# Optimization experiments

Hardware: AMD Instinct MI355X
Metric: run time of the kernel (lower is better)

Reference implementation:

```python
import jax, jax.numpy as jnp
import numpy as np

L = 15      # GNN layers
D = 128     # hidden width


def _mlp3(x, w1, b1, w2, b2, w3, b3):
    h = jax.nn.relu(x @ w1 + b1)
    h = jax.nn.relu(h @ w2 + b2)
    return h @ w3 + b3


def _layernorm(x, g, b, eps=1e-5):
    mu = x.mean(-1, keepdims=True)
    var = ((x - mu) ** 2).mean(-1, keepdims=True)
    return (x - mu) / jnp.sqrt(var + eps) * g + b


def _gather(V, idx):
    # V: [B,N,D], idx: [B,E] -> [B,E,D]
    return jax.vmap(lambda v, i: v[i])(V, idx)


def _scatter_sum(e, idx, n):
    # e: [B,E,D], idx: [B,E] -> [B,n,D]
    return jax.vmap(lambda ee, ii: jnp.zeros((n, ee.shape[-1]), ee.dtype).at[ii].add(ee))(e, idx)


def setup_inputs() -> dict:
    key = jax.random.key(0)
    ks = iter(jax.random.split(key, 64))
    B, N, Eg = 1, 10000, 40000

    def lin(fi, fo, pre=()):
        s = 1.0 / np.sqrt(fi)
        w = jax.random.uniform(next(ks), pre + (fi, fo), jnp.float32, -s, s)
        b = jax.random.uniform(next(ks), pre + (fo,), jnp.float32, -s, s)
        return w, b

    inp = {}
    inp['node_pos'] = jax.random.normal(next(ks), (B, N, 3), jnp.float32)
    inp['areas'] = jax.random.uniform(next(ks), (B, N, 1), jnp.float32)
    inp['info'] = jax.random.normal(next(ks), (B, 1, 8), jnp.float32)
    inp['edges'] = jax.random.randint(next(ks), (B, Eg, 2), 0, N, jnp.int32)

    # Encoder MLPs (layer_norm=True)
    for pre, fi in [('fv', 12), ('fe', 4)]:
        w1, b1 = lin(fi, D); w2, b2 = lin(D, D); w3, b3 = lin(D, D)
        inp[pre + '_w1'], inp[pre + '_b1'] = w1, b1
        inp[pre + '_w2'], inp[pre + '_b2'] = w2, b2
        inp[pre + '_w3'], inp[pre + '_b3'] = w3, b3
        inp[pre + '_g'] = jnp.ones((D,), jnp.float32)
        inp[pre + '_bt'] = jnp.zeros((D,), jnp.float32)

    # 15 GNN layers, stacked along leading axis (layer_norm=False)
    for pre, fi in [('ge', D + 2 * D), ('gn', D + D)]:
        w1, b1 = lin(fi, D, (L,)); w2, b2 = lin(D, D, (L,)); w3, b3 = lin(D, D, (L,))
        inp[pre + '_w1'], inp[pre + '_b1'] = w1, b1
        inp[pre + '_w2'], inp[pre + '_b2'] = w2, b2
        inp[pre + '_w3'], inp[pre + '_b3'] = w3, b3

    # Decoder (layer_norm=False, output_size=1)
    w1, b1 = lin(D, D); w2, b2 = lin(D, D); w3, b3 = lin(D, 1)
    inp['de_w1'], inp['de_b1'] = w1, b1
    inp['de_w2'], inp['de_b2'] = w2, b2
    inp['de_w3'], inp['de_b3'] = w3, b3
    return inp


def reference(node_pos, areas, info, edges,
              fv_w1, fv_b1, fv_w2, fv_b2, fv_w3, fv_b3, fv_g, fv_bt,
              fe_w1, fe_b1, fe_w2, fe_b2, fe_w3, fe_b3, fe_g, fe_bt,
              ge_w1, ge_b1, ge_w2, ge_b2, ge_w3, ge_b3,
              gn_w1, gn_b1, gn_w2, gn_b2, gn_w3, gn_b3,
              de_w1, de_b1, de_w2, de_b2, de_w3, de_b3):
    B, N, _ = node_pos.shape
    info_b = jnp.broadcast_to(info, (B, N, info.shape[-1]))
    en_in = jnp.concatenate([node_pos, areas, info_b], -1)  # [B,N,12]

    s, r = edges[..., 0], edges[..., 1]
    dist = _gather(node_pos, s) - _gather(node_pos, r)      # [B,E,3]
    nrm = jnp.sqrt((dist ** 2).sum(-1, keepdims=True))
    E_raw = jnp.concatenate([dist, nrm], -1)                # [B,E,4]

    V = _layernorm(_mlp3(en_in, fv_w1, fv_b1, fv_w2, fv_b2, fv_w3, fv_b3), fv_g, fv_bt)
    E = _layernorm(_mlp3(E_raw, fe_w1, fe_b1, fe_w2, fe_b2, fe_w3, fe_b3), fe_g, fe_bt)

    def step(carry, p):
        V, E = carry
        w1, b1, w2, b2, w3, b3, nw1, nb1, nw2, nb2, nw3, nb3 = p
        e_in = jnp.concatenate([_gather(V, s), _gather(V, r), E], -1)  # [B,E,384]
        e_emb = _mlp3(e_in, w1, b1, w2, b2, w3, b3)
        agg = _scatter_sum(e_emb, s, N)                                # [B,N,128]
        v_emb = _mlp3(jnp.concatenate([V, agg], -1), nw1, nb1, nw2, nb2, nw3, nb3)
        return (V + v_emb, E + e_emb), None

    (V, E), _ = jax.lax.scan(step, (V, E),
                             (ge_w1, ge_b1, ge_w2, ge_b2, ge_w3, ge_b3,
                              gn_w1, gn_b1, gn_w2, gn_b2, gn_w3, gn_b3))

    return _mlp3(V, de_w1, de_b1, de_w2, de_b2, de_w3, de_b3)  # [B,N,1]
```

## Files before the change

### kernel.cpp

```cpp
#include <hip/hip_runtime.h>

#define DD 128
#define N_NODE 10000
#define N_EDGE 40000
#define N_LAYER 15

typedef unsigned short U16;
typedef __attribute__((ext_vector_type(8))) short short8;
typedef __attribute__((ext_vector_type(4))) float f32x4;

enum { A_BF16 = 0, A_EDGE, A_NODE, A_ENCIN, A_ERAW };
enum { EPI_F = 0, EPI_EDGE, EPI_NODE, EPI_DEC };

#define OFF_FV1 0
#define OFF_FV2 4096
#define OFF_FV3 20480
#define OFF_FE1 36864
#define OFF_FE2 40960
#define OFF_FE3 57344
#define OFF_GE1 73728
#define OFF_GE2 811008
#define OFF_GE3 1056768
#define OFF_GN1 1302528
#define OFF_GN2 1794048
#define OFF_GN3 2039808
#define OFF_DE1 2285568
#define OFF_DE2 2301952
#define WT_TOTAL 2318336

static __device__ __forceinline__ U16 f2b(float f) {
    union { float f; unsigned u; } x; x.f = f;
    unsigned u = x.u;
    return (U16)((u + 0x7fffu + ((u >> 16) & 1u)) >> 16);
}
static __device__ __forceinline__ float b2f(U16 u) {
    union { unsigned u; float f; } x; x.u = ((unsigned)u) << 16;
    return x.f;
}

static __device__ __forceinline__ void wgb() {
    __asm__ __volatile__("s_waitcnt lgkmcnt(0)\n\ts_barrier" ::: "memory");
}

struct I4x2 { int4 a, b; };

__global__ __launch_bounds__(256)
void wprep(const float* fv1, const float* fv2, const float* fv3,
           const float* fe1, const float* fe2, const float* fe3,
           const float* ge1, const float* ge2, const float* ge3,
           const float* gn1, const float* gn2, const float* gn3,
           const float* de1, const float* de2, U16* Wt)
{
    int b = blockIdx.x;
    const float* src; U16* dst; int K, Kpad, k0;
    if      (b < 1)   { src = fv1; K = 12;  Kpad = 32;  dst = Wt + OFF_FV1; k0 = b * 32; }
    else if (b < 5)   { src = fv2; K = 128; Kpad = 128; dst = Wt + OFF_FV2; k0 = (b-1)*32; }
    else if (b < 9)   { src = fv3; K = 128; Kpad = 128; dst = Wt + OFF_FV3; k0 = (b-5)*32; }
    else if (b < 10)  { src = fe1; K = 4;   Kpad = 32;  dst = Wt + OFF_FE1; k0 = (b-9)*32; }
    else if (b < 14)  { src = fe2; K = 128; Kpad = 128; dst = Wt + OFF_FE2; k0 = (b-10)*32; }
    else if (b < 18)  { src = fe3; K = 128; Kpad = 128; dst = Wt + OFF_FE3; k0 = (b-14)*32; }
    else if (b < 198) { int r = b-18,  mi = r/12, s = r%12; src = ge1 + (size_t)mi*384*128; K = 384; Kpad = 384; dst = Wt + OFF_GE1 + (size_t)mi*49152; k0 = s*32; }
    else if (b < 258) { int r = b-198, mi = r/4,  s = r%4;  src = ge2 + (size_t)mi*16384;   K = 128; Kpad = 128; dst = Wt + OFF_GE2 + (size_t)mi*16384; k0 = s*32; }
    else if (b < 318) { int r = b-258, mi = r/4,  s = r%4;  src = ge3 + (size_t)mi*16384;   K = 128; Kpad = 128; dst = Wt + OFF_GE3 + (size_t)mi*16384; k0 = s*32; }
    else if (b < 438) { int r = b-318, mi = r/8,  s = r%8;  src = gn1 + (size_t)mi*32768;   K = 256; Kpad = 256; dst = Wt + OFF_GN1 + (size_t)mi*32768; k0 = s*32; }
    else if (b < 498) { int r = b-438, mi = r/4,  s = r%4;  src = gn2 + (size_t)mi*16384;   K = 128; Kpad = 128; dst = Wt + OFF_GN2 + (size_t)mi*16384; k0 = s*32; }
    else if (b < 558) { int r = b-498, mi = r/4,  s = r%4;  src = gn3 + (size_t)mi*16384;   K = 128; Kpad = 128; dst = Wt + OFF_GN3 + (size_t)mi*16384; k0 = s*32; }
    else if (b < 562) { src = de1; K = 128; Kpad = 128; dst = Wt + OFF_DE1; k0 = (b-558)*32; }
    else              { src = de2; K = 128; Kpad = 128; dst = Wt + OFF_DE2; k0 = (b-562)*32; }

    __shared__ float T[32][129];
    #pragma unroll
    for (int i = 0; i < 16; ++i) {
        int l = threadIdx.x + i * 256;
        int kk = l >> 7, n = l & 127;
        int kg = k0 + kk;
        T[kk][n] = (kg < K) ? src[(size_t)kg * 128 + n] : 0.f;
    }
    __syncthreads();
    int n = threadIdx.x >> 1, h = threadIdx.x & 1;
    union { U16 u[16]; int4 v[2]; } o;
    #pragma unroll
    for (int j = 0; j < 16; ++j) o.u[j] = f2b(T[h * 16 + j][n]);
    int4* d = (int4*)(dst + (size_t)n * Kpad + k0 + h * 16);
    d[0] = o.v[0]; d[1] = o.v[1];
}

__global__ __launch_bounds__(256)
void csr_hist(const int* __restrict__ edges, int* __restrict__ cnt, int Eg)
{
    int e = blockIdx.x * 256 + threadIdx.x;
    if (e < Eg) atomicAdd(&cnt[edges[2 * e]], 1);
}

__global__ __launch_bounds__(256)
void csr_scan(const int* __restrict__ cnt, int* __restrict__ rowptr,
              int* __restrict__ cursor, int n)
{
    __shared__ int ps[256];
    int t = threadIdx.x, base = t * 40;
    int s = 0;
    for (int j = 0; j < 40; ++j) if (base + j < n) s += cnt[base + j];
    ps[t] = s; __syncthreads();
    for (int off = 1; off < 256; off <<= 1) {
        int v = (t >= off) ? ps[t - off] : 0;
        __syncthreads();
        ps[t] += v;
        __syncthreads();
    }
    int run = ps[t] - s;
    for (int j = 0; j < 40; ++j) {
        if (base + j < n) {
            rowptr[base + j] = run;
            cursor[base + j] = run;
            run += cnt[base + j];
        }
    }
    if (t == 255) rowptr[n] = ps[255];
}

__global__ __launch_bounds__(256)
void csr_scatter(const int* __restrict__ edges, int* __restrict__ cursor,
                 int* __restrict__ spos, int Eg)
{
    int e = blockIdx.x * 256 + threadIdx.x;
    if (e < Eg) spos[e] = atomicAdd(&cursor[edges[2 * e]], 1);
}

template<int ASRC, int EPI, int K1>
__global__ __launch_bounds__(256)
void mlp3(const U16* __restrict__ Af,
          const U16* __restrict__ W1, const float* __restrict__ b1,
          const U16* __restrict__ W2, const float* __restrict__ b2,
          const U16* __restrict__ W3, const float* __restrict__ b3,
          U16* __restrict__ outh, float* __restrict__ outf,
          const int* __restrict__ edges, const int* __restrict__ rowptr,
          const int* __restrict__ spos, float* __restrict__ eEs,
          const U16* __restrict__ Vh, const U16* __restrict__ Ehp,
          const float* __restrict__ pos, const float* __restrict__ area,
          const float* __restrict__ info, const float* __restrict__ w3f,
          int M)
{
    __shared__ U16 As[2][64][40];
    __shared__ U16 Bs[2][128][40];
    __shared__ U16 Hs[64][132];

    const int tid  = threadIdx.x;
    const int row0 = blockIdx.x * 64;
    const int wave = tid >> 6, lane = tid & 63;
    const int quad = lane >> 4, l16 = lane & 15;
    const int wm = (wave >> 1) * 32;
    const int wn = (wave & 1) * 64;
    const int sr = tid >> 2, sh = tid & 3;
    const int br = tid >> 1, bh = tid & 1;
    const int sm = row0 + sr;
    const bool valid = (sm < M);

    int si = 0, ri = 0, jbeg = 0, jend = 0;
    if ((ASRC == A_EDGE || ASRC == A_ERAW) && valid) {
        si = edges[2 * sm]; ri = edges[2 * sm + 1];
    }
    if (ASRC == A_NODE && valid) { jbeg = rowptr[sm]; jend = rowptr[sm + 1]; }

    f32x4 acc[4][2];

    auto zacc = [&] {
        #pragma unroll
        for (int i = 0; i < 4; ++i)
            #pragma unroll
            for (int j = 0; j < 2; ++j) acc[i][j] = (f32x4)0.f;
    };

    auto ldA = [&](int c) -> int4 {
        if (ASRC == A_ENCIN || ASRC == A_ERAW) {
            union { U16 u[8]; int4 v; } pk;
            #pragma unroll
            for (int j = 0; j < 8; ++j) pk.u[j] = 0;
            if (valid) {
                if (ASRC == A_ENCIN) {
                    #pragma unroll
                    for (int j = 0; j < 8; ++j) {
                        int col = sh * 8 + j;
                        float x = 0.f;
                        if (col < 3)       x = pos[3 * sm + col];
                        else if (col == 3) x = area[sm];
                        else if (col < 12) x = info[col - 4];
                        pk.u[j] = f2b(x);
                    }
                } else if (sh == 0) {
                    float dx = pos[3*si]   - pos[3*ri];
                    float dy = pos[3*si+1] - pos[3*ri+1];
                    float dz = pos[3*si+2] - pos[3*ri+2];
                    float nm = sqrtf(dx*dx + dy*dy + dz*dz);
                    pk.u[0] = f2b(dx); pk.u[1] = f2b(dy);
                    pk.u[2] = f2b(dz); pk.u[3] = f2b(nm);
                }
            }
            return pk.v;
        } else if (ASRC == A_NODE && c >= 4) {
            float a[8];
            #pragma unroll
            for (int i = 0; i < 8; ++i) a[i] = 0.f;
            if (valid) {
                const float* base = eEs + (c - 4) * 32 + sh * 8;
                for (int j = jbeg; j < jend; ++j) {
                    const float4* r = (const float4*)(base + (size_t)j * 128);
                    float4 x0 = r[0], x1 = r[1];
                    a[0]+=x0.x; a[1]+=x0.y; a[2]+=x0.z; a[3]+=x0.w;
                    a[4]+=x1.x; a[5]+=x1.y; a[6]+=x1.z; a[7]+=x1.w;
                }
            }
            union { U16 u[8]; int4 v; } pk;
            #pragma unroll
            for (int i = 0; i < 8; ++i) pk.u[i] = f2b(a[i]);
            return pk.v;
        } else {
            const U16* s;
            if (ASRC == A_BF16)        s = Af + (size_t)sm * K1 + c * 32;
            else if (ASRC == A_EDGE) {
                if (c < 4)             s = Vh  + (size_t)si * 128 + c * 32;
                else if (c < 8)        s = Vh  + (size_t)ri * 128 + (c - 4) * 32;
                else                   s = Ehp + (size_t)sm * 128 + (c - 8) * 32;
            } else                     s = Vh  + (size_t)sm * 128 + c * 32;
            return valid ? *(const int4*)(s + sh * 8) : make_int4(0,0,0,0);
        }
    };

    auto ldW = [&](const U16* W, int Kw, int c) -> I4x2 {
        const U16* s = W + (size_t)br * Kw + c * 32 + bh * 16;
        I4x2 r;
        r.a = ((const int4*)s)[0];
        r.b = ((const int4*)s)[1];
        return r;
    };

    auto wrA = [&](int b, int4 v) { *(int4*)&As[b][sr][sh * 8] = v; };
    auto wrW = [&](int b, I4x2 w) {
        *(int4*)&Bs[b][br][bh * 16]     = w.a;
        *(int4*)&Bs[b][br][bh * 16 + 8] = w.b;
    };

    auto mfA = [&](int b) {
        short8 wf[4], af[2];
        #pragma unroll
        for (int g = 0; g < 4; ++g)
            wf[g] = *(const short8*)&Bs[b][wn + g*16 + l16][quad * 8];
        #pragma unroll
        for (int g = 0; g < 2; ++g)
            af[g] = *(const short8*)&As[b][wm + g*16 + l16][quad * 8];
        #pragma unroll
        for (int wg = 0; wg < 4; ++wg)
            #pragma unroll
            for (int ag = 0; ag < 2; ++ag)
                acc[wg][ag] = __builtin_amdgcn_mfma_f32_16x16x32_bf16(
                    wf[wg], af[ag], acc[wg][ag], 0, 0, 0);
    };

    auto mfH = [&](int c, int b) {
        short8 wf[4], af[2];
        #pragma unroll
        for (int g = 0; g < 4; ++g)
            wf[g] = *(const short8*)&Bs[b][wn + g*16 + l16][quad * 8];
        #pragma unroll
        for (int g = 0; g < 2; ++g)
            af[g] = *(const short8*)&Hs[wm + g*16 + l16][c * 32 + quad * 8];
        #pragma unroll
        for (int wg = 0; wg < 4; ++wg)
            #pragma unroll
            for (int ag = 0; ag < 2; ++ag)
                acc[wg][ag] = __builtin_amdgcn_mfma_f32_16x16x32_bf16(
                    wf[wg], af[ag], acc[wg][ag], 0, 0, 0);
    };

    auto hwrite = [&](const float* bias) {
        #pragma unroll
        for (int wg = 0; wg < 4; ++wg) {
            f32x4 bv = *(const f32x4*)&bias[wn + wg*16 + quad*4];
            #pragma unroll
            for (int ag = 0; ag < 2; ++ag) {
                int m  = wm + ag*16 + l16;
                int n0 = wn + wg*16 + quad*4;
                union { U16 u[4]; uint2 q; } pk;
                #pragma unroll
                for (int rg = 0; rg < 4; ++rg)
                    pk.u[rg] = f2b(fmaxf(acc[wg][ag][rg] + bv[rg], 0.f));
                *(uint2*)&Hs[m][n0] = pk.q;
            }
        }
    };

    int4 ra0, ra1; I4x2 rw0, rw1;
    constexpr int C1 = K1 / 32;

    zacc();
    ra0 = ldA(0); rw0 = ldW(W1, K1, 0);
    if (C1 > 1) { ra1 = ldA(1); rw1 = ldW(W1, K1, 1); }
    wrA(0, ra0); wrW(0, rw0);
    wgb();
    #pragma unroll
    for (int c = 0; c < C1; ++c) {
        if (c + 2 < C1) {
            if ((c & 1) == 0) { ra0 = ldA(c + 2); rw0 = ldW(W1, K1, c + 2); }
            else              { ra1 = ldA(c + 2); rw1 = ldW(W1, K1, c + 2); }
        }
        if (c + 1 < C1) {
            if (((c + 1) & 1) == 0) { wrA(0, ra0); wrW(0, rw0); }
            else                    { wrA(1, ra1); wrW(1, rw1); }
        }
        mfA(c & 1);
        wgb();
    }

    rw0 = ldW(W2, 128, 0); rw1 = ldW(W2, 128, 1);
    hwrite(b1);
    wgb();
    zacc();
    wrW(0, rw0);
    wgb();
    #pragma unroll
    for (int c = 0; c < 4; ++c) {
        if (c + 2 < 4) {
            if ((c & 1) == 0) rw0 = ldW(W2, 128, c + 2);
            else              rw1 = ldW(W2, 128, c + 2);
        }
        if (c + 1 < 4) {
            if (((c + 1) & 1) == 0) wrW(0, rw0);
            else                    wrW(1, rw1);
        }
        mfH(c, c & 1);
        wgb();
    }

    if (EPI == EPI_DEC) {
        hwrite(b2);
        wgb();
        int mg = row0 + sr;
        float v = 0.f;
        if (mg < M) {
            const U16* hr = &Hs[sr][sh * 32];
            const float* wr = w3f + sh * 32;
            #pragma unroll
            for (int j = 0; j < 32; ++j) v += b2f(hr[j]) * wr[j];
        }
        v += __shfl_xor(v, 1);
        v += __shfl_xor(v, 2);
        if (sh == 0 && mg < M) outf[mg] = v + b3[0];
        return;
    }

    rw0 = ldW(W3, 128, 0); rw1 = ldW(W3, 128, 1);
    hwrite(b2);
    wgb();
    zacc();
    wrW(0, rw0);
    wgb();
    #pragma unroll
    for (int c = 0; c < 4; ++c) {
        if (c + 2 < 4) {
            if ((c & 1) == 0) rw0 = ldW(W3, 128, c + 2);
            else              rw1 = ldW(W3, 128, c + 2);
        }
        if (c + 1 < 4) {
            if (((c + 1) & 1) == 0) wrW(0, rw0);
            else                    wrW(1, rw1);
        }
        mfH(c, c & 1);
        wgb();
    }

    f32x4 bvs[4];
    #pragma unroll
    for (int wg = 0; wg < 4; ++wg)
        bvs[wg] = *(const f32x4*)&b3[wn + wg*16 + quad*4];
    #pragma unroll
    for (int ag = 0; ag < 2; ++ag) {
        int mg = row0 + wm + ag*16 + l16;
        if (mg >= M) continue;
        int sp = 0;
        if (EPI == EPI_EDGE) sp = spos[mg];
        #pragma unroll
        for (int wg = 0; wg < 4; ++wg) {
            int n0 = wn + wg*16 + quad*4;
            f32x4 v;
            #pragma unroll
            for (int rg = 0; rg < 4; ++rg) v[rg] = acc[wg][ag][rg] + bvs[wg][rg];
            size_t o = (size_t)mg * 128 + n0;
            if (EPI == EPI_F) {
                *(f32x4*)&outf[o] = v;
            } else {
                f32x4 c = *(f32x4*)&outf[o];
                c += v;
                *(f32x4*)&outf[o] = c;
                union { U16 u[4]; uint2 q; } pk;
                #pragma unroll
                for (int rg = 0; rg < 4; ++rg) pk.u[rg] = f2b(c[rg]);
                *(uint2*)&outh[o] = pk.q;
                if (EPI == EPI_EDGE)
                    *(f32x4*)&eEs[(size_t)sp * 128 + n0] = v;
            }
        }
    }
}

__global__ __launch_bounds__(256)
void ln_kernel(float* __restrict__ X, const float* __restrict__ g,
               const float* __restrict__ b, U16* __restrict__ Xh, int rows)
{
    int row  = blockIdx.x * 4 + (threadIdx.x >> 6);
    int lane = threadIdx.x & 63;
    if (row >= rows) return;
    float x0 = X[row * DD + lane];
    float x1 = X[row * DD + 64 + lane];
    float s = x0 + x1, q = x0 * x0 + x1 * x1;
    #pragma unroll
    for (int off = 32; off; off >>= 1) {
        s += __shfl_xor(s, off);
        q += __shfl_xor(q, off);
    }
    float mu  = s * (1.f / 128.f);
    float var = q * (1.f / 128.f) - mu * mu;
    float inv = rsqrtf(var + 1e-5f);
    float y0 = (x0 - mu) * inv * g[lane]      + b[lane];
    float y1 = (x1 - mu) * inv * g[64 + lane] + b[64 + lane];
    X[row * DD + lane]       = y0;
    X[row * DD + 64 + lane]  = y1;
    Xh[row * DD + lane]      = f2b(y0);
    Xh[row * DD + 64 + lane] = f2b(y1);
}

extern "C" void kernel_launch(void* const* d_in, const int* in_sizes, int n_in,
                              void* d_out, int out_size, void* d_ws, size_t ws_size,
                              hipStream_t stream)
{
    (void)in_sizes; (void)n_in; (void)out_size; (void)ws_size;

    const float* pos   = (const float*)d_in[0];
    const float* area  = (const float*)d_in[1];
    const float* info  = (const float*)d_in[2];
    const int*   edges = (const int*)d_in[3];
    const float* fv_w1 = (const float*)d_in[4];
    const float* fv_b1 = (const float*)d_in[5];
    const float* fv_w2 = (const float*)d_in[6];
    const float* fv_b2 = (const float*)d_in[7];
    const float* fv_w3 = (const float*)d_in[8];
    const float* fv_b3 = (const float*)d_in[9];
    const float* fv_g  = (const float*)d_in[10];
    const float* fv_bt = (const float*)d_in[11];
    const float* fe_w1 = (const float*)d_in[12];
    const float* fe_b1 = (const float*)d_in[13];
    const float* fe_w2 = (const float*)d_in[14];
    const float* fe_b2 = (const float*)d_in[15];
    const float* fe_w3 = (const float*)d_in[16];
    const float* fe_b3 = (const float*)d_in[17];
    const float* fe_g  = (const float*)d_in[18];
    const float* fe_bt = (const float*)d_in[19];
    const float* ge_w1 = (const float*)d_in[20];
    const float* ge_b1 = (const float*)d_in[21];
    const float* ge_w2 = (const float*)d_in[22];
    const float* ge_b2 = (const float*)d_in[23];
    const float* ge_w3 = (const float*)d_in[24];
    const float* ge_b3 = (const float*)d_in[25];
    const float* gn_w1 = (const float*)d_in[26];
    const float* gn_b1 = (const float*)d_in[27];
    const float* gn_w2 = (const float*)d_in[28];
    const float* gn_b2 = (const float*)d_in[29];
    const float* gn_w3 = (const float*)d_in[30];
    const float* gn_b3 = (const float*)d_in[31];
    const float* de_w1 = (const float*)d_in[32];
    const float* de_b1 = (const float*)d_in[33];
    const float* de_w2 = (const float*)d_in[34];
    const float* de_b2 = (const float*)d_in[35];
    const float* de_w3 = (const float*)d_in[36];
    const float* de_b3 = (const float*)d_in[37];

    char* p = (char*)d_ws;
    float* Vf   = (float*)p;  p += (size_t)N_NODE * 128 * 4;
    float* Ef   = (float*)p;  p += (size_t)N_EDGE * 128 * 4;
    float* eEs  = (float*)p;  p += (size_t)N_EDGE * 128 * 4;
    U16*  Vh    = (U16*)p;    p += (size_t)N_NODE * 128 * 2;
    U16*  Eh    = (U16*)p;    p += (size_t)N_EDGE * 128 * 2;
    U16*  Wt    = (U16*)p;    p += (size_t)WT_TOTAL * 2;
    int*  rowptr = (int*)p;   p += (size_t)(N_NODE + 4) * 4;
    int*  cursor = (int*)p;   p += (size_t)N_NODE * 4;
    int*  cnt    = (int*)p;   p += (size_t)N_NODE * 4;
    int*  spos   = (int*)p;   p += (size_t)N_EDGE * 4;

    const int gbE = (N_EDGE + 63) / 64;
    const int gbN = (N_NODE + 63) / 64;

    wprep<<<566, 256, 0, stream>>>(fv_w1, fv_w2, fv_w3, fe_w1, fe_w2, fe_w3,
                                   ge_w1, ge_w2, ge_w3, gn_w1, gn_w2, gn_w3,
                                   de_w1, de_w2, Wt);
    hipMemsetAsync(cnt, 0, (size_t)N_NODE * 4, stream);
    csr_hist<<<(N_EDGE + 255) / 256, 256, 0, stream>>>(edges, cnt, N_EDGE);
    csr_scan<<<1, 256, 0, stream>>>(cnt, rowptr, cursor, N_NODE);
    csr_scatter<<<(N_EDGE + 255) / 256, 256, 0, stream>>>(edges, cursor, spos, N_EDGE);

    mlp3<A_ERAW, EPI_F, 32><<<gbE, 256, 0, stream>>>(
        nullptr, Wt + OFF_FE1, fe_b1, Wt + OFF_FE2, fe_b2, Wt + OFF_FE3, fe_b3,
        nullptr, Ef, edges, nullptr, nullptr, nullptr, nullptr, nullptr,
        pos, nullptr, nullptr, nullptr, N_EDGE);
    ln_kernel<<<(N_EDGE + 3) / 4, 256, 0, stream>>>(Ef, fe_g, fe_bt, Eh, N_EDGE);

    mlp3<A_ENCIN, EPI_F, 32><<<gbN, 256, 0, stream>>>(
        nullptr, Wt + OFF_FV1, fv_b1, Wt + OFF_FV2, fv_b2, Wt + OFF_FV3, fv_b3,
        nullptr, Vf, nullptr, nullptr, nullptr, nullptr, nullptr, nullptr,
        pos, area, info, nullptr, N_NODE);
    ln_kernel<<<(N_NODE + 3) / 4, 256, 0, stream>>>(Vf, fv_g, fv_bt, Vh, N_NODE);

    for (int l = 0; l < N_LAYER; ++l) {
        mlp3<A_EDGE, EPI_EDGE, 384><<<gbE, 256, 0, stream>>>(
            nullptr,
            Wt + OFF_GE1 + (size_t)l * 49152, ge_b1 + (size_t)l * 128,
            Wt + OFF_GE2 + (size_t)l * 16384, ge_b2 + (size_t)l * 128,
            Wt + OFF_GE3 + (size_t)l * 16384, ge_b3 + (size_t)l * 128,
            Eh, Ef, edges, nullptr, spos, eEs, Vh, Eh,
            nullptr, nullptr, nullptr, nullptr, N_EDGE);
        mlp3<A_NODE, EPI_NODE, 256><<<gbN, 256, 0, stream>>>(
            nullptr,
            Wt + OFF_GN1 + (size_t)l * 32768, gn_b1 + (size_t)l * 128,
            Wt + OFF_GN2 + (size_t)l * 16384, gn_b2 + (size_t)l * 128,
            Wt + OFF_GN3 + (size_t)l * 16384, gn_b3 + (size_t)l * 128,
            Vh, Vf, nullptr, rowptr, nullptr, eEs, Vh, nullptr,
            nullptr, nullptr, nullptr, nullptr, N_NODE);
    }

    mlp3<A_BF16, EPI_DEC, 128><<<gbN, 256, 0, stream>>>(
        Vh, Wt + OFF_DE1, de_b1, Wt + OFF_DE2, de_b2, nullptr, de_b3,
        nullptr, (float*)d_out, nullptr, nullptr, nullptr, nullptr, nullptr, nullptr,
        nullptr, nullptr, nullptr, de_w3, N_NODE);
}
```

Before: 1.094 ms.

## Move MLP kernels to 512-thread blocks and shrink node tiles to 32 rows

Each fused MLP block now runs 8 waves instead of 4, with the wave grid changed to 2x4 over a BM x 128 tile so each wave does fewer MFMAs per K-chunk. The row tile is templated: edge kernels keep 64 rows, while node, encoder and decoder kernels use 32 rows, doubling their grid size. The aim is more waves in flight to hide gather and global-load latency, and better CU fill for the 10k-node kernels. The cost is less weight reuse per block, extra barrier participants, and some threads left idle when staging A tiles.

After: 1.027 ms (median of 2 runs). 1.06x faster.

```diff
diff --git a/kernel.cpp b/kernel.cpp
--- a/kernel.cpp
+++ b/kernel.cpp
@@ -41,8 +41,6 @@
 static __device__ __forceinline__ void wgb() {
     __asm__ __volatile__("s_waitcnt lgkmcnt(0)\n\ts_barrier" ::: "memory");
 }
-
-struct I4x2 { int4 a, b; };
 
 __global__ __launch_bounds__(256)
 void wprep(const float* fv1, const float* fv2, const float* fv3,
@@ -126,8 +124,8 @@
     if (e < Eg) spos[e] = atomicAdd(&cursor[edges[2 * e]], 1);
 }
 
-template<int ASRC, int EPI, int K1>
-__global__ __launch_bounds__(256)
+template<int ASRC, int EPI, int K1, int BM>
+__global__ __launch_bounds__(512, 4)
 void mlp3(const U16* __restrict__ Af,
           const U16* __restrict__ W1, const float* __restrict__ b1,
           const U16* __restrict__ W2, const float* __restrict__ b2,
@@ -140,20 +138,22 @@
           const float* __restrict__ info, const float* __restrict__ w3f,
           int M)
 {
-    __shared__ U16 As[2][64][40];
+    constexpr int NAG = BM / 32;
+    __shared__ U16 As[2][BM][40];
     __shared__ U16 Bs[2][128][40];
-    __shared__ U16 Hs[64][132];
+    __shared__ U16 Hs[BM][132];
 
     const int tid  = threadIdx.x;
-    const int row0 = blockIdx.x * 64;
+    const int row0 = blockIdx.x * BM;
     const int wave = tid >> 6, lane = tid & 63;
     const int quad = lane >> 4, l16 = lane & 15;
-    const int wm = (wave >> 1) * 32;
-    const int wn = (wave & 1) * 64;
+    const int wm = (wave >> 2) * (16 * NAG);
+    const int wn = (wave & 3) * 32;
     const int sr = tid >> 2, sh = tid & 3;
-    const int br = tid >> 1, bh = tid & 1;
+    const int br = tid >> 2, bh = tid & 3;
     const int sm = row0 + sr;
-    const bool valid = (sm < M);
+    const bool stager = (tid < BM * 4);
+    const bool valid  = stager && (sm < M);
 
     int si = 0, ri = 0, jbeg = 0, jend = 0;
     if ((ASRC == A_EDGE || ASRC == A_ERAW) && valid) {
@@ -161,13 +161,13 @@
     }
     if (ASRC == A_NODE && valid) { jbeg = rowptr[sm]; jend = rowptr[sm + 1]; }
 
-    f32x4 acc[4][2];
+    f32x4 acc[2][NAG];
 
     auto zacc = [&] {
         #pragma unroll
-        for (int i = 0; i < 4; ++i)
-            #pragma unroll
-            for (int j = 0; j < 2; ++j) acc[i][j] = (f32x4)0.f;
+        for (int i = 0; i < 2; ++i)
+            #pragma unroll
+            for (int j = 0; j < NAG; ++j) acc[i][j] = (f32x4)0.f;
     };
 
     auto ldA = [&](int c) -> int4 {
@@ -225,58 +225,52 @@
         }
     };
 
-    auto ldW = [&](const U16* W, int Kw, int c) -> I4x2 {
-        const U16* s = W + (size_t)br * Kw + c * 32 + bh * 16;
-        I4x2 r;
-        r.a = ((const int4*)s)[0];
-        r.b = ((const int4*)s)[1];
-        return r;
+    auto ldW = [&](const U16* W, int Kw, int c) -> int4 {
+        const U16* s = W + (size_t)br * Kw + c * 32 + bh * 8;
+        return *(const int4*)s;
     };
 
-    auto wrA = [&](int b, int4 v) { *(int4*)&As[b][sr][sh * 8] = v; };
-    auto wrW = [&](int b, I4x2 w) {
-        *(int4*)&Bs[b][br][bh * 16]     = w.a;
-        *(int4*)&Bs[b][br][bh * 16 + 8] = w.b;
-    };
+    auto wrA = [&](int b, int4 v) { if (stager) *(int4*)&As[b][sr][sh * 8] = v; };
+    auto wrW = [&](int b, int4 w) { *(int4*)&Bs[b][br][bh * 8] = w; };
 
     auto mfA = [&](int b) {
-        short8 wf[4], af[2];
-        #pragma unroll
-        for (int g = 0; g < 4; ++g)
+        short8 wf[2], af[NAG];
+        #pragma unroll
+        for (int g = 0; g < 2; ++g)
             wf[g] = *(const short8*)&Bs[b][wn + g*16 + l16][quad * 8];
         #pragma unroll
-        for (int g = 0; g < 2; ++g)
+        for (int g = 0; g < NAG; ++g)
             af[g] = *(const short8*)&As[b][wm + g*16 + l16][quad * 8];
         #pragma unroll
-        for (int wg = 0; wg < 4; ++wg)
-            #pragma unroll
-            for (int ag = 0; ag < 2; ++ag)
+        for (int wg = 0; wg < 2; ++wg)
+            #pragma unroll
+            for (int ag = 0; ag < NAG; ++ag)
                 acc[wg][ag] = __builtin_amdgcn_mfma_f32_16x16x32_bf16(
                     wf[wg], af[ag], acc[wg][ag], 0, 0, 0);
     };
 
     auto mfH = [&](int c, int b) {
-        short8 wf[4], af[2];
-        #pragma unroll
-        for (int g = 0; g < 4; ++g)
+        short8 wf[2], af[NAG];
+        #pragma unroll
+        for (int g = 0; g < 2; ++g)
             wf[g] = *(const short8*)&Bs[b][wn + g*16 + l16][quad * 8];
         #pragma unroll
-        for (int g = 0; g < 2; ++g)
+        for (int g = 0; g < NAG; ++g)
             af[g] = *(const short8*)&Hs[wm + g*16 + l16][c * 32 + quad * 8];
         #pragma unroll
-        for (int wg = 0; wg < 4; ++wg)
-            #pragma unroll
-            for (int ag = 0; ag < 2; ++ag)
+        for (int wg = 0; wg < 2; ++wg)
+            #pragma unroll
+            for (int ag = 0; ag < NAG; ++ag)
                 acc[wg][ag] = __builtin_amdgcn_mfma_f32_16x16x32_bf16(
                     wf[wg], af[ag], acc[wg][ag], 0, 0, 0);
     };
 
     auto hwrite = [&](const float* bias) {
         #pragma unroll
-        for (int wg = 0; wg < 4; ++wg) {
+        for (int wg = 0; wg < 2; ++wg) {
             f32x4 bv = *(const f32x4*)&bias[wn + wg*16 + quad*4];
             #pragma unroll
-            for (int ag = 0; ag < 2; ++ag) {
+            for (int ag = 0; ag < NAG; ++ag) {
                 int m  = wm + ag*16 + l16;
                 int n0 = wn + wg*16 + quad*4;
                 union { U16 u[4]; uint2 q; } pk;
@@ -288,7 +282,7 @@
         }
     };
 
-    int4 ra0, ra1; I4x2 rw0, rw1;
+    int4 ra0, ra1, rw0, rw1;
     constexpr int C1 = K1 / 32;
 
     zacc();
@@ -333,17 +327,20 @@
     if (EPI == EPI_DEC) {
         hwrite(b2);
         wgb();
-        int mg = row0 + sr;
+        constexpr int TPR = 512 / BM;
+        constexpr int CPT = 128 / TPR;
+        int r = tid / TPR, s8 = tid % TPR;
+        int mg = row0 + r;
         float v = 0.f;
         if (mg < M) {
-            const U16* hr = &Hs[sr][sh * 32];
-            const float* wr = w3f + sh * 32;
-            #pragma unroll
-            for (int j = 0; j < 32; ++j) v += b2f(hr[j]) * wr[j];
-        }
-        v += __shfl_xor(v, 1);
-        v += __shfl_xor(v, 2);
-        if (sh == 0 && mg < M) outf[mg] = v + b3[0];
+            const U16* hr = &Hs[r][s8 * CPT];
+            const float* wr = w3f + s8 * CPT;
+            #pragma unroll
+            for (int j = 0; j < CPT; ++j) v += b2f(hr[j]) * wr[j];
+        }
+        #pragma unroll
+        for (int off = 1; off < TPR; off <<= 1) v += __shfl_xor(v, off);
+        if (s8 == 0 && mg < M) outf[mg] = v + b3[0];
         return;
     }
 
@@ -367,18 +364,18 @@
         wgb();
     }
 
-    f32x4 bvs[4];
-    #pragma unroll
-    for (int wg = 0; wg < 4; ++wg)
+    f32x4 bvs[2];
+    #pragma unroll
+    for (int wg = 0; wg < 2; ++wg)
         bvs[wg] = *(const f32x4*)&b3[wn + wg*16 + quad*4];
     #pragma unroll
-    for (int ag = 0; ag < 2; ++ag) {
+    for (int ag = 0; ag < NAG; ++ag) {
         int mg = row0 + wm + ag*16 + l16;
         if (mg >= M) continue;
         int sp = 0;
         if (EPI == EPI_EDGE) sp = spos[mg];
         #pragma unroll
-        for (int wg = 0; wg < 4; ++wg) {
+        for (int wg = 0; wg < 2; ++wg) {
             int n0 = wn + wg*16 + quad*4;
             f32x4 v;
             #pragma unroll
@@ -484,8 +481,8 @@
     int*  cnt    = (int*)p;   p += (size_t)N_NODE * 4;
     int*  spos   = (int*)p;   p += (size_t)N_EDGE * 4;
 
-    const int gbE = (N_EDGE + 63) / 64;
-    const int gbN = (N_NODE + 63) / 64;
+    const int gbE   = (N_EDGE + 63) / 64;
+    const int gbN32 = (N_NODE + 31) / 32;
 
     wprep<<<566, 256, 0, stream>>>(fv_w1, fv_w2, fv_w3, fe_w1, fe_w2, fe_w3,
                                    ge_w1, ge_w2, ge_w3, gn_w1, gn_w2, gn_w3,
@@ -495,27 +492,27 @@
     csr_scan<<<1, 256, 0, stream>>>(cnt, rowptr, cursor, N_NODE);
     csr_scatter<<<(N_EDGE + 255) / 256, 256, 0, stream>>>(edges, cursor, spos, N_EDGE);
 
-    mlp3<A_ERAW, EPI_F, 32><<<gbE, 256, 0, stream>>>(
+    mlp3<A_ERAW, EPI_F, 32, 64><<<gbE, 512, 0, stream>>>(
         nullptr, Wt + OFF_FE1, fe_b1, Wt + OFF_FE2, fe_b2, Wt + OFF_FE3, fe_b3,
         nullptr, Ef, edges, nullptr, nullptr, nullptr, nullptr, nullptr,
         pos, nullptr, nullptr, nullptr, N_EDGE);
     ln_kernel<<<(N_EDGE + 3) / 4, 256, 0, stream>>>(Ef, fe_g, fe_bt, Eh, N_EDGE);
 
-    mlp3<A_ENCIN, EPI_F, 32><<<gbN, 256, 0, stream>>>(
+    mlp3<A_ENCIN, EPI_F, 32, 32><<<gbN32, 512, 0, stream>>>(
         nullptr, Wt + OFF_FV1, fv_b1, Wt + OFF_FV2, fv_b2, Wt + OFF_FV3, fv_b3,
         nullptr, Vf, nullptr, nullptr, nullptr, nullptr, nullptr, nullptr,
         pos, area, info, nullptr, N_NODE);
     ln_kernel<<<(N_NODE + 3) / 4, 256, 0, stream>>>(Vf, fv_g, fv_bt, Vh, N_NODE);
 
     for (int l = 0; l < N_LAYER; ++l) {
-        mlp3<A_EDGE, EPI_EDGE, 384><<<gbE, 256, 0, stream>>>(
+        mlp3<A_EDGE, EPI_EDGE, 384, 64><<<gbE, 512, 0, stream>>>(
             nullptr,
             Wt + OFF_GE1 + (size_t)l * 49152, ge_b1 + (size_t)l * 128,
             Wt + OFF_GE2 + (size_t)l * 16384, ge_b2 + (size_t)l * 128,
             Wt + OFF_GE3 + (size_t)l * 16384, ge_b3 + (size_t)l * 128,
             Eh, Ef, edges, nullptr, spos, eEs, Vh, Eh,
             nullptr, nullptr, nullptr, nullptr, N_EDGE);
-        mlp3<A_NODE, EPI_NODE, 256><<<gbN, 256, 0, stream>>>(
+        mlp3<A_NODE, EPI_NODE, 256, 32><<<gbN32, 512, 0, stream>>>(
             nullptr,
             Wt + OFF_GN1 + (size_t)l * 32768, gn_b1 + (size_t)l * 128,
             Wt + OFF_GN2 + (size_t)l * 16384, gn_b2 + (size_t)l * 128,
@@ -524,7 +521,7 @@
             nullptr, nullptr, nullptr, nullptr, N_NODE);
     }
 
-    mlp3<A_BF16, EPI_DEC, 128><<<gbN, 256, 0, stream>>>(
+    mlp3<A_BF16, EPI_DEC, 128, 32><<<gbN32, 512, 0, stream>>>(
         Vh, Wt + OFF_DE1, de_b1, Wt + OFF_DE2, de_b2, nullptr, de_b3,
         nullptr, (float*)d_out, nullptr, nullptr, nullptr, nullptr, nullptr, nullptr,
         nullptr, nullptr, nullptr, de_w3, N_NODE);
```
